# Kernel tuning notes

Hardware: AMD Instinct MI355X
Metric: run time of the kernel (lower is better)

## Reference

```python
import jax, jax.numpy as jnp
import numpy as np

B, N, D = 2, 2048, 1024
H, DH = 16, 64
THETA = 10000.0


def setup_inputs() -> dict:
    key = jax.random.key(0)
    k1, k2, k3, k4 = jax.random.split(key, 4)
    hidden_states = jax.random.normal(k1, (B, N, D), dtype=jnp.float32)
    # to_qkv: Linear(D, 3*H*DH, bias=False); stored as [in, out]
    w_qkv = jax.random.normal(k2, (D, 3 * H * DH), dtype=jnp.float32) * (1.0 / np.sqrt(D))
    # to_out: Linear(H*DH, D) with bias (torch default)
    w_out = jax.random.normal(k3, (H * DH, D), dtype=jnp.float32) * (1.0 / np.sqrt(H * DH))
    b_out = jax.random.normal(k4, (D,), dtype=jnp.float32) * 0.01
    return {"hidden_states": hidden_states, "w_qkv": w_qkv, "w_out": w_out, "b_out": b_out}


def _rope_cos_sin(n, dh, dtype):
    # lucidrains RotaryEmbedding: interleaved pairs, theta=10000
    inv_freq = 1.0 / (THETA ** (jnp.arange(0, dh, 2, dtype=jnp.float32) / dh))  # [dh/2]
    t = jnp.arange(n, dtype=jnp.float32)
    freqs = t[:, None] * inv_freq[None, :]                 # [n, dh/2]
    freqs = jnp.repeat(freqs, 2, axis=-1)                  # [n, dh] interleaved
    return jnp.cos(freqs).astype(dtype), jnp.sin(freqs).astype(dtype)


def _rotate_half(x):
    # interleaved: (..., d) -> pairs (x1, x2) -> (-x2, x1)
    x = x.reshape(*x.shape[:-1], -1, 2)
    x1, x2 = x[..., 0], x[..., 1]
    return jnp.stack([-x2, x1], axis=-1).reshape(*x.shape[:-2], -1)


def reference(hidden_states, w_qkv, w_out, b_out):
    b, n, d = hidden_states.shape
    qkv = hidden_states @ w_qkv                            # [b, n, 3*H*DH]
    q, k, v = jnp.split(qkv, 3, axis=-1)
    # b n (h d) -> b h n d
    to_heads = lambda t: t.reshape(b, n, H, DH).transpose(0, 2, 1, 3)
    q, k, v = to_heads(q), to_heads(k), to_heads(v)
    cos, sin = _rope_cos_sin(n, DH, q.dtype)               # [n, DH]
    q = q * cos + _rotate_half(q) * sin
    k = k * cos + _rotate_half(k) * sin
    scale = 1.0 / np.sqrt(DH)
    scores = jnp.einsum('bhqd,bhkd->bhqk', q, k) * scale   # [b, h, n, n]
    attn = jax.nn.softmax(scores, axis=-1)
    out = jnp.einsum('bhqk,bhkd->bhqd', attn, v)           # [b, h, n, DH]
    out = out.transpose(0, 2, 1, 3).reshape(b, n, H * DH)  # b h n d -> b n (h d)
    return out @ w_out + b_out
```

## Files before the change

### kernel.cpp

```cpp
#include <hip/hip_runtime.h>
#include <hip/hip_bf16.h>

typedef __bf16 bf16;
typedef unsigned int u32;
typedef __attribute__((ext_vector_type(4))) float f32x4;
typedef __attribute__((ext_vector_type(16))) float f32x16;
typedef __attribute__((ext_vector_type(8))) bf16 bf16x8;
typedef __attribute__((ext_vector_type(4))) bf16 bf16x4;
typedef __attribute__((ext_vector_type(2))) bf16 bf16x2;
typedef __attribute__((ext_vector_type(4))) u32 u32x4;
typedef __attribute__((ext_vector_type(2))) u32 u32x2;

#define GPTR(p) ((const __attribute__((address_space(1))) u32*)(p))
#define SPTR(p) ((__attribute__((address_space(3))) u32*)(p))

#if __has_builtin(__builtin_amdgcn_permlane32_swap)
#define HAVE_PLSWAP 1
#else
#define HAVE_PLSWAP 0
#endif
#if __has_builtin(__builtin_amdgcn_fdot2_f32_bf16)
#define HAVE_DOT2 1
#else
#define HAVE_DOT2 0
#endif

constexpr int BATCH = 2, SEQ = 2048, DMODEL = 1024, NH = 16, HD = 64, QKV3 = 3072;
constexpr int MTOK = BATCH * SEQ;

constexpr size_t OXB = 0;
constexpr size_t OWQ = OXB + (size_t)MTOK * DMODEL * 2;
constexpr size_t OWO = OWQ + (size_t)QKV3 * DMODEL * 2;
constexpr size_t OCS = OWO + (size_t)DMODEL * DMODEL * 2;
constexpr size_t OCQ = OCS + (size_t)SEQ * 32 * 8;
constexpr size_t OQR = OCQ + (size_t)MTOK * QKV3 * 2;
constexpr size_t OKR = OQR + (size_t)BATCH * NH * SEQ * HD * 2;
constexpr size_t OVT = OKR + (size_t)BATCH * NH * SEQ * HD * 2;
constexpr size_t OAO = OXB;

static __device__ __forceinline__ bf16 tobf(float x) { return (bf16)x; }
static __device__ __forceinline__ float tof(bf16 x) { return (float)x; }

static __device__ __forceinline__ f32x4 mfma16(bf16x8 a, bf16x8 b, f32x4 c) {
  return __builtin_amdgcn_mfma_f32_16x16x32_bf16(a, b, c, 0, 0, 0);
}
static __device__ __forceinline__ f32x16 mfma32(bf16x8 a, bf16x8 b, f32x16 c) {
  return __builtin_amdgcn_mfma_f32_32x32x16_bf16(a, b, c, 0, 0, 0);
}

__global__ void k_prep(const float* __restrict__ hs, const float* __restrict__ wqkv,
                       const float* __restrict__ wout, float* __restrict__ cs,
                       bf16* __restrict__ Xb, bf16* __restrict__ Wqkt,
                       bf16* __restrict__ Woutt) {
  __shared__ float tile[32][33];
  int blk = blockIdx.x, tid = threadIdx.x;
  if (blk < 256) {
    int idx = blk * 256 + tid;
    int n = idx >> 5, i = idx & 31;
    float freq = powf(10000.0f, -(float)(2 * i) / 64.0f);
    float ang = (float)n * freq;
    float s, c;
    sincosf(ang, &s, &c);
    cs[idx * 2] = c;
    cs[idx * 2 + 1] = s;
  } else if (blk < 256 + 4096) {
    int i = (blk - 256) * 256 + tid;
    float4 v = ((const float4*)hs)[i];
    bf16x4 o = {tobf(v.x), tobf(v.y), tobf(v.z), tobf(v.w)};
    ((bf16x4*)Xb)[i] = o;
  } else {
    const float* in;
    bf16* out;
    int R, C, n0, k0;
    if (blk < 256 + 4096 + 3072) {
      int t = blk - 4352;
      in = wqkv; out = Wqkt; R = DMODEL; C = QKV3;
      n0 = (t % 96) * 32; k0 = (t / 96) * 32;
    } else {
      int t = blk - 7424;
      in = wout; out = Woutt; R = DMODEL; C = DMODEL;
      n0 = (t & 31) * 32; k0 = (t >> 5) * 32;
    }
    int tx = tid & 31, ty = tid >> 5;
#pragma unroll
    for (int r = ty; r < 32; r += 8) tile[r][tx] = in[(size_t)(k0 + r) * C + n0 + tx];
    __syncthreads();
#pragma unroll
    for (int r = ty; r < 32; r += 8) out[(size_t)(n0 + r) * R + k0 + tx] = tobf(tile[tx][r]);
  }
}


__global__ __launch_bounds__(256) void k_gemm2(const bf16* __restrict__ A, const bf16* __restrict__ Bt,
                                               float* __restrict__ C, const float* __restrict__ bias,
                                               int M, int Nn, int K) {
  __shared__ __attribute__((aligned(16))) char smem[49152];
  const int nTn = Nn >> 7;
  int nwg = gridDim.x;
  int bid = blockIdx.x;
  int wgs = (bid & 7) * (nwg >> 3) + (bid >> 3);
  const int m0 = (wgs / nTn) << 7;
  const int n0 = (wgs % nTn) << 7;
  const int tid = threadIdx.x;
  const int lane = tid & 63, w = tid >> 6;
  const int wr = w >> 1, wc = w & 1;
  const int l15 = lane & 15, lhi = lane >> 4;
  f32x4 acc[4][4] = {};

  const int flat0 = w * 1024 + lane * 16;
  const int flat1 = flat0 + 4096;
  const int row0 = flat0 >> 6, ke0 = (flat0 & 63) >> 1;
  const int row1 = flat1 >> 6, ke1 = (flat1 & 63) >> 1;

#define GSTAGE(bb_, k0_)                                                                       \
  do {                                                                                         \
    __builtin_amdgcn_global_load_lds(GPTR(A + (size_t)(m0 + row0) * K + (k0_) + ke0),          \
                                     SPTR(smem + (bb_)*16384 + flat0), 16, 0, 0);              \
    __builtin_amdgcn_global_load_lds(GPTR(A + (size_t)(m0 + row1) * K + (k0_) + ke1),          \
                                     SPTR(smem + (bb_)*16384 + flat1), 16, 0, 0);              \
    __builtin_amdgcn_global_load_lds(GPTR(Bt + (size_t)(n0 + row0) * K + (k0_) + ke0),         \
                                     SPTR(smem + (bb_)*16384 + 8192 + flat0), 16, 0, 0);       \
    __builtin_amdgcn_global_load_lds(GPTR(Bt + (size_t)(n0 + row1) * K + (k0_) + ke1),         \
                                     SPTR(smem + (bb_)*16384 + 8192 + flat1), 16, 0, 0);       \
  } while (0)

  GSTAGE(0, 0);
  GSTAGE(1, 32);
  const int nIt = K >> 5;
  int bi = 0, b2 = 2;
  for (int it = 0; it < nIt; ++it) {
    if (it < nIt - 1) {
      asm volatile("s_waitcnt vmcnt(4)" ::: "memory");
    } else {
      asm volatile("s_waitcnt vmcnt(0)" ::: "memory");
    }
    __builtin_amdgcn_s_barrier();
    if (it + 2 < nIt) GSTAGE(b2, (it + 2) << 5);
    const bf16* As = (const bf16*)(smem + bi * 16384);
    const bf16* Bs = (const bf16*)(smem + bi * 16384 + 8192);
    bf16x8 af[4], bfv[4];
#pragma unroll
    for (int i = 0; i < 4; ++i) {
      af[i] = *(const bf16x8*)(As + (wr * 64 + i * 16 + l15) * 32 + lhi * 8);
      bfv[i] = *(const bf16x8*)(Bs + (wc * 64 + i * 16 + l15) * 32 + lhi * 8);
    }
    __builtin_amdgcn_s_setprio(1);
#pragma unroll
    for (int i = 0; i < 4; ++i)
#pragma unroll
      for (int j = 0; j < 4; ++j) acc[i][j] = mfma16(af[i], bfv[j], acc[i][j]);
    __builtin_amdgcn_s_setprio(0);
    bi = (bi == 2) ? 0 : bi + 1;
    b2 = (b2 == 2) ? 0 : b2 + 1;
  }
#undef GSTAGE

  float bj[4];
#pragma unroll
  for (int j = 0; j < 4; ++j) bj[j] = bias[n0 + wc * 64 + j * 16 + l15];
#pragma unroll
  for (int i = 0; i < 4; ++i)
#pragma unroll
    for (int j = 0; j < 4; ++j) {
      int row = m0 + wr * 64 + i * 16 + lhi * 4;
      int col = n0 + wc * 64 + j * 16 + l15;
#pragma unroll
      for (int r = 0; r < 4; ++r) C[(size_t)(row + r) * Nn + col] = acc[i][j][r] + bj[j];
    }
}


__global__ __launch_bounds__(256) void k_gemm1f(const bf16* __restrict__ A, const bf16* __restrict__ Bt,
                                                const float* __restrict__ cs,
                                                bf16* __restrict__ Qr, bf16* __restrict__ Kr,
                                                bf16* __restrict__ Vt) {
  constexpr int K = DMODEL, Nn = QKV3;
  __shared__ __attribute__((aligned(16))) char smem[49152];
  const int nTn = Nn >> 7;
  int nwg = gridDim.x;
  int bid = blockIdx.x;
  int wgs = (bid & 7) * (nwg >> 3) + (bid >> 3);
  const int m0 = (wgs / nTn) << 7;
  const int n0 = (wgs % nTn) << 7;
  const int tid = threadIdx.x;
  const int lane = tid & 63, w = tid >> 6;
  const int wr = w >> 1, wc = w & 1;
  const int l15 = lane & 15, lhi = lane >> 4;
  f32x4 acc[4][4] = {};

  const int flat0 = w * 1024 + lane * 16;
  const int flat1 = flat0 + 4096;
  const int row0 = flat0 >> 6, ke0 = (flat0 & 63) >> 1;
  const int row1 = flat1 >> 6, ke1 = (flat1 & 63) >> 1;

#define GSTAGE(bb_, k0_)                                                                       \
  do {                                                                                         \
    __builtin_amdgcn_global_load_lds(GPTR(A + (size_t)(m0 + row0) * K + (k0_) + ke0),          \
                                     SPTR(smem + (bb_)*16384 + flat0), 16, 0, 0);              \
    __builtin_amdgcn_global_load_lds(GPTR(A + (size_t)(m0 + row1) * K + (k0_) + ke1),          \
                                     SPTR(smem + (bb_)*16384 + flat1), 16, 0, 0);              \
    __builtin_amdgcn_global_load_lds(GPTR(Bt + (size_t)(n0 + row0) * K + (k0_) + ke0),         \
                                     SPTR(smem + (bb_)*16384 + 8192 + flat0), 16, 0, 0);       \
    __builtin_amdgcn_global_load_lds(GPTR(Bt + (size_t)(n0 + row1) * K + (k0_) + ke1),         \
                                     SPTR(smem + (bb_)*16384 + 8192 + flat1), 16, 0, 0);       \
  } while (0)

  GSTAGE(0, 0);
  GSTAGE(1, 32);
  const int nIt = K >> 5;
  int bi = 0, b2 = 2;
  for (int it = 0; it < nIt; ++it) {
    if (it < nIt - 1) {
      asm volatile("s_waitcnt vmcnt(4)" ::: "memory");
    } else {
      asm volatile("s_waitcnt vmcnt(0)" ::: "memory");
    }
    __builtin_amdgcn_s_barrier();
    if (it + 2 < nIt) GSTAGE(b2, (it + 2) << 5);
    const bf16* As = (const bf16*)(smem + bi * 16384);
    const bf16* Bs = (const bf16*)(smem + bi * 16384 + 8192);
    bf16x8 af[4], bfv[4];
#pragma unroll
    for (int i = 0; i < 4; ++i) {
      af[i] = *(const bf16x8*)(As + (wr * 64 + i * 16 + l15) * 32 + lhi * 8);
      bfv[i] = *(const bf16x8*)(Bs + (wc * 64 + i * 16 + l15) * 32 + lhi * 8);
    }
    __builtin_amdgcn_s_setprio(1);
#pragma unroll
    for (int i = 0; i < 4; ++i)
#pragma unroll
      for (int j = 0; j < 4; ++j) acc[i][j] = mfma16(af[i], bfv[j], acc[i][j]);
    __builtin_amdgcn_s_setprio(0);
    bi = (bi == 2) ? 0 : bi + 1;
    b2 = (b2 == 2) ? 0 : b2 + 1;
  }
#undef GSTAGE

  __syncthreads();
  const int part = n0 >> 10;
  const int b = m0 >> 11;

  if (part < 2) {
    bf16* Cs = (bf16*)smem;
#pragma unroll
    for (int i = 0; i < 4; ++i)
#pragma unroll
      for (int j = 0; j < 4; ++j) {
        int row = wr * 64 + i * 16 + lhi * 4;
        int col = wc * 64 + j * 16 + l15;
#pragma unroll
        for (int r = 0; r < 4; ++r) Cs[(row + r) * 128 + col] = tobf(acc[i][j][r]);
      }
    __syncthreads();
    bf16* dst = part == 0 ? Qr : Kr;
#pragma unroll
    for (int inst = 0; inst < 8; ++inst) {
      int flat = inst * 4096 + tid * 16;
      int row = flat >> 8, c0 = (flat & 255) >> 1;
      int n = (m0 + row) & 2047;
      int gc = (n0 & 1023) + c0;
      int h = gc >> 6, d0 = gc & 63;
      u32x4 v = *(const u32x4*)(smem + flat);
      const float* cp = cs + (((n << 5) + (d0 >> 1)) << 1);
      f32x4 csA = *(const f32x4*)cp;
      f32x4 csB = *(const f32x4*)(cp + 4);
      u32x4 ow;
#pragma unroll
      for (int j = 0; j < 4; ++j) {
        float cc = (j == 0) ? csA[0] : (j == 1) ? csA[2] : (j == 2) ? csB[0] : csB[2];
        float sn = (j == 0) ? csA[1] : (j == 1) ? csA[3] : (j == 2) ? csB[1] : csB[3];
        u32 pw = v[j];
        u32 tl = pw << 16, th = pw & 0xffff0000u;
        float a0, a1;
        __builtin_memcpy(&a0, &tl, 4);
        __builtin_memcpy(&a1, &th, 4);
        bf16 o0 = tobf(a0 * cc - a1 * sn);
        bf16 o1 = tobf(a1 * cc + a0 * sn);
        unsigned short u0, u1;
        __builtin_memcpy(&u0, &o0, 2);
        __builtin_memcpy(&u1, &o1, 2);
        ow[j] = (u32)u0 | ((u32)u1 << 16);
      }
      *(u32x4*)(dst + (((size_t)(b * 16 + h) * 2048 + n) << 6) + d0) = ow;
    }
  } else {
#pragma unroll
    for (int i = 0; i < 4; ++i)
#pragma unroll
      for (int j = 0; j < 4; ++j) {
        int col = wc * 64 + j * 16 + l15;
#pragma unroll
        for (int r = 0; r < 4; ++r) {
          int row = wr * 64 + i * 16 + lhi * 4 + r;
          int byte = (col << 8) + ((((row >> 3) ^ (col & 7)) << 4) | ((row & 7) << 1));
          *(bf16*)(smem + byte) = tobf(acc[i][j][r]);
        }
      }
    __syncthreads();
#pragma unroll
    for (int inst = 0; inst < 8; ++inst) {
      int flat = inst * 4096 + tid * 16;
      int c = flat >> 8;
      int rr0 = (flat & 255) >> 1;
      u32x4 vv = *(const u32x4*)(smem + (c << 8) + ((((rr0 >> 3) ^ (c & 7)) << 4)));
      int gc = (n0 & 1023) + c;
      int h = gc >> 6, dd = gc & 63;
      *(u32x4*)(Vt + (((size_t)(b * 16 + h) * 64 + dd) << 11) + (m0 & 2047) + rr0) = vv;
    }
  }
}

__global__ __launch_bounds__(512, 4) void k_attn(const bf16* __restrict__ Qr,
                                                 const bf16* __restrict__ Kr,
                                                 const bf16* __restrict__ Vt,
                                                 bf16* __restrict__ AO) {
  __shared__ __attribute__((aligned(16))) char lds[2][40960];
  int wg = blockIdx.x;
  int work = (wg & 7) * 64 + (wg >> 3);
  int qc = work & 15, h = (work >> 4) & 15, b = work >> 8;
  int tid = threadIdx.x;
  int wv = tid >> 6, lane = tid & 63;
  int pipe = wv >> 2, wsub = wv & 3;
  int l31 = lane & 31, h5 = lane >> 5;
  int q0 = qc * 128 + wsub * 32;
  int kbase = pipe << 10;
  const bf16* Qb = Qr + ((size_t)(b * NH + h)) * SEQ * 64;
  const bf16* Kb = Kr + ((size_t)(b * NH + h)) * SEQ * 64;
  const bf16* Vb = Vt + ((size_t)(b * NH + h)) * 64 * SEQ;
  char* pb = lds[pipe];

  int ptid = tid & 255;
  int sf0 = ptid * 16, sf1 = 4096 + ptid * 16;
  int sr0 = sf0 >> 7, sr1 = sf1 >> 7;
  int sc0 = (sf0 & 127) ^ ((sr0 & 7) << 4);
  int sc1 = (sf1 & 127) ^ ((sr1 & 7) << 4);
  size_t kgb0 = (size_t)sr0 * 64 + (sc0 >> 1), kgb1 = (size_t)sr1 * 64 + (sc1 >> 1);
  size_t vgb0 = (size_t)sr0 * SEQ + (sc0 >> 1), vgb1 = (size_t)sr1 * SEQ + (sc1 >> 1);

#define STAGE_K(bi_, kb_)                                                                     \
  do {                                                                                        \
    size_t ko_ = (size_t)(kbase + (kb_));                                                     \
    char* bb_ = pb + (bi_)*8192;                                                              \
    __builtin_amdgcn_global_load_lds(GPTR(Kb + ko_ * 64 + kgb0), SPTR(bb_ + sf0), 16, 0, 0);  \
    __builtin_amdgcn_global_load_lds(GPTR(Kb + ko_ * 64 + kgb1), SPTR(bb_ + sf1), 16, 0, 0);  \
  } while (0)
#define STAGE_V(bi_, kb_)                                                                     \
  do {                                                                                        \
    size_t ko_ = (size_t)(kbase + (kb_));                                                     \
    char* bb_ = pb + 24576 + (bi_)*8192;                                                      \
    __builtin_amdgcn_global_load_lds(GPTR(Vb + ko_ + vgb0), SPTR(bb_ + sf0), 16, 0, 0);       \
    __builtin_amdgcn_global_load_lds(GPTR(Vb + ko_ + vgb1), SPTR(bb_ + sf1), 16, 0, 0);       \
  } while (0)

  bf16x8 qf[4];
#pragma unroll
  for (int s = 0; s < 4; ++s) qf[s] = *(const bf16x8*)(Qb + (q0 + l31) * 64 + s * 16 + h5 * 8);

  f32x16 acc0 = {}, acc1 = {};
#if HAVE_DOT2
  float sacc0 = 0.f, sacc1 = 0.f, sacc2 = 0.f, sacc3 = 0.f;
  const bf16x2 ones2 = {(bf16)1.0f, (bf16)1.0f};
#else
  float ssum_run = 0.f;
#endif
  const float sc = 0.125f * 1.44269504f;
  const float FOFF = 8.0f;
  const int sw = (l31 & 7) << 4;
  const int cbase = h5 * 16;

  STAGE_K(0, 0);
  STAGE_V(0, 0);
  STAGE_K(1, 64);

  constexpr int NT = (SEQ / 2) / 64;
  int kc = 0, kc2 = 2;
  for (int t = 0; t < NT; ++t) {
    if (t < NT - 1) {
      asm volatile("s_waitcnt vmcnt(2)" ::: "memory");
    } else {
      asm volatile("s_waitcnt vmcnt(0)" ::: "memory");
    }
    __builtin_amdgcn_s_barrier();
    if (t + 1 < NT) STAGE_V((t + 1) & 1, (t + 1) * 64);
    if (t + 2 < NT) STAGE_K(kc2, (t + 2) * 64);
    char* cbK = pb + kc * 8192;
    char* cbV = pb + 24576 + (t & 1) * 8192;
    kc = (kc == 2) ? 0 : kc + 1;
    kc2 = (kc2 == 2) ? 0 : kc2 + 1;

    f32x16 st0 = {}, st1 = {};
    __builtin_amdgcn_s_setprio(1);
#pragma unroll
    for (int s = 0; s < 4; ++s) {
      bf16x8 kf0 = *(const bf16x8*)(cbK + l31 * 128 + ((s * 32 + cbase) ^ sw));
      bf16x8 kf1 = *(const bf16x8*)(cbK + 4096 + l31 * 128 + ((s * 32 + cbase) ^ sw));
      st0 = mfma32(kf0, qf[s], st0);
      st1 = mfma32(kf1, qf[s], st1);
    }
    __builtin_amdgcn_s_setprio(0);

    float p[32];
#pragma unroll
    for (int r = 0; r < 16; ++r) p[r] = __builtin_amdgcn_exp2f(fmaf(st0[r], sc, -FOFF));
#pragma unroll
    for (int r = 0; r < 16; ++r) p[16 + r] = __builtin_amdgcn_exp2f(fmaf(st1[r], sc, -FOFF));

    u32 P32[16];
#pragma unroll
    for (int i = 0; i < 16; ++i) {
      bf16 lo = tobf(p[2 * i]), hi = tobf(p[2 * i + 1]);
      unsigned short ul, uh;
      __builtin_memcpy(&ul, &lo, 2);
      __builtin_memcpy(&uh, &hi, 2);
      P32[i] = (u32)ul | ((u32)uh << 16);
    }

#if HAVE_DOT2
#pragma unroll
    for (int i = 0; i < 16; i += 4) {
      sacc0 = __builtin_amdgcn_fdot2_f32_bf16(__builtin_bit_cast(bf16x2, P32[i]), ones2, sacc0, false);
      sacc1 = __builtin_amdgcn_fdot2_f32_bf16(__builtin_bit_cast(bf16x2, P32[i + 1]), ones2, sacc1, false);
      sacc2 = __builtin_amdgcn_fdot2_f32_bf16(__builtin_bit_cast(bf16x2, P32[i + 2]), ones2, sacc2, false);
      sacc3 = __builtin_amdgcn_fdot2_f32_bf16(__builtin_bit_cast(bf16x2, P32[i + 3]), ones2, sacc3, false);
    }
#else
    {
      float sm[16];
#pragma unroll
      for (int i = 0; i < 16; ++i) {
        u32 ulo = P32[i] << 16, uhi = P32[i] & 0xffff0000u;
        float flo, fhi;
        __builtin_memcpy(&flo, &ulo, 4);
        __builtin_memcpy(&fhi, &uhi, 4);
        sm[i] = flo + fhi;
      }
#pragma unroll
      for (int off = 8; off > 0; off >>= 1)
#pragma unroll
        for (int r = 0; r < off; ++r) sm[r] += sm[r + off];
      ssum_run += sm[0];
    }
#endif

#if !HAVE_PLSWAP
    const int evens[8] = {0, 1, 4, 5, 8, 9, 12, 13};
    const int odds[8] = {2, 3, 6, 7, 10, 11, 14, 15};
    u32 recv[8];
#pragma unroll
    for (int j = 0; j < 8; ++j) {
      u32 sv = h5 ? P32[evens[j]] : P32[odds[j]];
      recv[j] = (u32)__shfl_xor((int)sv, 32, 64);
    }
#endif

    __builtin_amdgcn_s_setprio(1);
#pragma unroll
    for (int s2 = 0; s2 < 4; ++s2) {
      int x0 = ((s2 >> 1) << 3) + ((s2 & 1) << 2);
#if HAVE_PLSWAP
      u32x2 r02 = __builtin_amdgcn_permlane32_swap(P32[x0], P32[x0 + 2], false, false);
      u32x2 r13 = __builtin_amdgcn_permlane32_swap(P32[x0 + 1], P32[x0 + 3], false, false);
      u32x4 wv4 = {r02.x, r13.x, r02.y, r13.y};
#else
      u32 w0 = h5 ? recv[2 * s2] : P32[x0];
      u32 w1 = h5 ? recv[2 * s2 + 1] : P32[x0 + 1];
      u32 w2 = h5 ? P32[x0 + 2] : recv[2 * s2];
      u32 w3 = h5 ? P32[x0 + 3] : recv[2 * s2 + 1];
      u32x4 wv4 = {w0, w1, w2, w3};
#endif
      bf16x8 pfr = __builtin_bit_cast(bf16x8, wv4);
      bf16x8 vf0 = *(const bf16x8*)(cbV + l31 * 128 + ((s2 * 32 + cbase) ^ sw));
      bf16x8 vf1 = *(const bf16x8*)(cbV + 4096 + l31 * 128 + ((s2 * 32 + cbase) ^ sw));
      acc0 = mfma32(vf0, pfr, acc0);
      acc1 = mfma32(vf1, pfr, acc1);
    }
    __builtin_amdgcn_s_setprio(0);
  }

#if HAVE_DOT2
  float ssum = (sacc0 + sacc1) + (sacc2 + sacc3);
#else
  float ssum = ssum_run;
#endif

  __syncthreads();
  float* cacc = (float*)&lds[0][0];
  float* csum = (float*)(&lds[0][0] + 36864);
  int slot = (wsub * 64 + lane) * 36;
  if (pipe == 1) {
#pragma unroll
    for (int r = 0; r < 16; r += 4) {
      *(f32x4*)(cacc + slot + r) = f32x4{acc0[r], acc0[r + 1], acc0[r + 2], acc0[r + 3]};
      *(f32x4*)(cacc + slot + 16 + r) = f32x4{acc1[r], acc1[r + 1], acc1[r + 2], acc1[r + 3]};
    }
    csum[wsub * 64 + lane] = ssum;
  }
  __syncthreads();
  if (pipe == 0) {
#pragma unroll
    for (int r = 0; r < 16; r += 4) {
      f32x4 v0 = *(const f32x4*)(cacc + slot + r);
      f32x4 v1 = *(const f32x4*)(cacc + slot + 16 + r);
#pragma unroll
      for (int j = 0; j < 4; ++j) { acc0[r + j] += v0[j]; acc1[r + j] += v1[j]; }
    }
    ssum += csum[wsub * 64 + lane];
    ssum += __shfl_xor(ssum, 32, 64);
    float inv = 1.0f / ssum;
    size_t tok = (size_t)(b * SEQ + q0 + l31);
#pragma unroll
    for (int a = 0; a < 4; ++a) {
      bf16x4 ov0, ov1;
#pragma unroll
      for (int j = 0; j < 4; ++j) {
        ov0[j] = tobf(acc0[4 * a + j] * inv);
        ov1[j] = tobf(acc1[4 * a + j] * inv);
      }
      *(bf16x4*)(AO + tok * (NH * HD) + h * 64 + 8 * a + 4 * h5) = ov0;
      *(bf16x4*)(AO + tok * (NH * HD) + h * 64 + 32 + 8 * a + 4 * h5) = ov1;
    }
  }
#undef STAGE_K
#undef STAGE_V
}


extern "C" void kernel_launch(void* const* d_in, const int* in_sizes, int n_in,
                              void* d_out, int out_size, void* d_ws, size_t ws_size,
                              hipStream_t stream) {
  const float* hs = (const float*)d_in[0];
  const float* wqkv = (const float*)d_in[1];
  const float* wout = (const float*)d_in[2];
  const float* bout = (const float*)d_in[3];
  char* ws = (char*)d_ws;
  bf16* Xb = (bf16*)(ws + OXB);
  bf16* Wqkt = (bf16*)(ws + OWQ);
  bf16* Woutt = (bf16*)(ws + OWO);
  float* cs = (float*)(ws + OCS);
  bf16* Qr = (bf16*)(ws + OQR);
  bf16* Kr = (bf16*)(ws + OKR);
  bf16* Vt = (bf16*)(ws + OVT);
  bf16* AO = (bf16*)(ws + OAO);

  k_prep<<<8448, 256, 0, stream>>>(hs, wqkv, wout, cs, Xb, Wqkt, Woutt);
  k_gemm1f<<<(MTOK / 128) * (QKV3 / 128), 256, 0, stream>>>(Xb, Wqkt, cs, Qr, Kr, Vt);
  k_attn<<<BATCH * NH * (SEQ / 128), 512, 0, stream>>>(Qr, Kr, Vt, AO);
  k_gemm2<<<(MTOK / 128) * (DMODEL / 128), 256, 0, stream>>>(AO, Woutt, (float*)d_out, bout, MTOK, DMODEL, DMODEL);
}
```

Measured before the change: 117.6 us.

## Swizzle GEMM LDS layout and move w_out transpose into QKV GEMM launch

Applies an XOR swizzle to the 16-byte chunks of each LDS row in both GEMM kernels, at the global-to-LDS write and at the fragment read, to reduce LDS bank conflicts. Moves the w_out fp32->bf16 transpose out of the prep kernel into extra trailing blocks of the QKV GEMM launch. This shortens the prep kernel's critical path and lets the transpose overlap the GEMM tail. It adds index arithmetic, and the extra blocks enlarge the GEMM grid.

Result: no change. 116.2 us (-1.2%).

```diff
diff --git a/kernel.cpp b/kernel.cpp
--- a/kernel.cpp
+++ b/kernel.cpp
@@ -49,9 +49,8 @@
 }
 
 __global__ void k_prep(const float* __restrict__ hs, const float* __restrict__ wqkv,
-                       const float* __restrict__ wout, float* __restrict__ cs,
-                       bf16* __restrict__ Xb, bf16* __restrict__ Wqkt,
-                       bf16* __restrict__ Woutt) {
+                       float* __restrict__ cs, bf16* __restrict__ Xb,
+                       bf16* __restrict__ Wqkt) {
   __shared__ float tile[32][33];
   int blk = blockIdx.x, tid = threadIdx.x;
   if (blk < 256) {
@@ -69,26 +68,17 @@
     bf16x4 o = {tobf(v.x), tobf(v.y), tobf(v.z), tobf(v.w)};
     ((bf16x4*)Xb)[i] = o;
   } else {
-    const float* in;
-    bf16* out;
-    int R, C, n0, k0;
-    if (blk < 256 + 4096 + 3072) {
-      int t = blk - 4352;
-      in = wqkv; out = Wqkt; R = DMODEL; C = QKV3;
-      n0 = (t % 96) * 32; k0 = (t / 96) * 32;
-    } else {
-      int t = blk - 7424;
-      in = wout; out = Woutt; R = DMODEL; C = DMODEL;
-      n0 = (t & 31) * 32; k0 = (t >> 5) * 32;
-    }
+    int t = blk - 4352;
+    int n0 = (t % 96) * 32, k0 = (t / 96) * 32;
     int tx = tid & 31, ty = tid >> 5;
 #pragma unroll
-    for (int r = ty; r < 32; r += 8) tile[r][tx] = in[(size_t)(k0 + r) * C + n0 + tx];
+    for (int r = ty; r < 32; r += 8) tile[r][tx] = wqkv[(size_t)(k0 + r) * QKV3 + n0 + tx];
     __syncthreads();
 #pragma unroll
-    for (int r = ty; r < 32; r += 8) out[(size_t)(n0 + r) * R + k0 + tx] = tobf(tile[tx][r]);
-  }
-}
+    for (int r = ty; r < 32; r += 8) Wqkt[(size_t)(n0 + r) * DMODEL + k0 + tx] = tobf(tile[tx][r]);
+  }
+}
+
 
 
 __global__ __launch_bounds__(256) void k_gemm2(const bf16* __restrict__ A, const bf16* __restrict__ Bt,
@@ -109,8 +99,10 @@
 
   const int flat0 = w * 1024 + lane * 16;
   const int flat1 = flat0 + 4096;
-  const int row0 = flat0 >> 6, ke0 = (flat0 & 63) >> 1;
-  const int row1 = flat1 >> 6, ke1 = (flat1 & 63) >> 1;
+  const int row0 = flat0 >> 6, row1 = flat1 >> 6;
+  const int ke0 = (((flat0 & 63) >> 4) ^ ((row0 >> 1) & 3)) << 3;
+  const int ke1 = (((flat1 & 63) >> 4) ^ ((row1 >> 1) & 3)) << 3;
+  const int rsw = ((l15 >> 1) & 3) << 3;
 
 #define GSTAGE(bb_, k0_)                                                                       \
   do {                                                                                         \
@@ -141,8 +133,8 @@
     bf16x8 af[4], bfv[4];
 #pragma unroll
     for (int i = 0; i < 4; ++i) {
-      af[i] = *(const bf16x8*)(As + (wr * 64 + i * 16 + l15) * 32 + lhi * 8);
-      bfv[i] = *(const bf16x8*)(Bs + (wc * 64 + i * 16 + l15) * 32 + lhi * 8);
+      af[i] = *(const bf16x8*)(As + (wr * 64 + i * 16 + l15) * 32 + ((lhi << 3) ^ rsw));
+      bfv[i] = *(const bf16x8*)(Bs + (wc * 64 + i * 16 + l15) * 32 + ((lhi << 3) ^ rsw));
     }
     __builtin_amdgcn_s_setprio(1);
 #pragma unroll
@@ -172,17 +164,32 @@
 
 __global__ __launch_bounds__(256) void k_gemm1f(const bf16* __restrict__ A, const bf16* __restrict__ Bt,
                                                 const float* __restrict__ cs,
+                                                const float* __restrict__ wout, bf16* __restrict__ Woutt,
                                                 bf16* __restrict__ Qr, bf16* __restrict__ Kr,
                                                 bf16* __restrict__ Vt) {
   constexpr int K = DMODEL, Nn = QKV3;
+  constexpr int NG = (MTOK / 128) * (QKV3 / 128);
   __shared__ __attribute__((aligned(16))) char smem[49152];
+  int bid = blockIdx.x;
+  const int tid = threadIdx.x;
+
+  if (bid >= NG) {
+    float* tile = (float*)smem;
+    int t = bid - NG;
+    int n0 = (t & 31) * 32, k0 = (t >> 5) * 32;
+    int tx = tid & 31, ty = tid >> 5;
+#pragma unroll
+    for (int r = ty; r < 32; r += 8) tile[r * 33 + tx] = wout[(size_t)(k0 + r) * DMODEL + n0 + tx];
+    __syncthreads();
+#pragma unroll
+    for (int r = ty; r < 32; r += 8) Woutt[(size_t)(n0 + r) * DMODEL + k0 + tx] = tobf(tile[tx * 33 + r]);
+    return;
+  }
+
   const int nTn = Nn >> 7;
-  int nwg = gridDim.x;
-  int bid = blockIdx.x;
-  int wgs = (bid & 7) * (nwg >> 3) + (bid >> 3);
+  int wgs = (bid & 7) * (NG >> 3) + (bid >> 3);
   const int m0 = (wgs / nTn) << 7;
   const int n0 = (wgs % nTn) << 7;
-  const int tid = threadIdx.x;
   const int lane = tid & 63, w = tid >> 6;
   const int wr = w >> 1, wc = w & 1;
   const int l15 = lane & 15, lhi = lane >> 4;
@@ -190,8 +197,10 @@
 
   const int flat0 = w * 1024 + lane * 16;
   const int flat1 = flat0 + 4096;
-  const int row0 = flat0 >> 6, ke0 = (flat0 & 63) >> 1;
-  const int row1 = flat1 >> 6, ke1 = (flat1 & 63) >> 1;
+  const int row0 = flat0 >> 6, row1 = flat1 >> 6;
+  const int ke0 = (((flat0 & 63) >> 4) ^ ((row0 >> 1) & 3)) << 3;
+  const int ke1 = (((flat1 & 63) >> 4) ^ ((row1 >> 1) & 3)) << 3;
+  const int rsw = ((l15 >> 1) & 3) << 3;
 
 #define GSTAGE(bb_, k0_)                                                                       \
   do {                                                                                         \
@@ -222,8 +231,8 @@
     bf16x8 af[4], bfv[4];
 #pragma unroll
     for (int i = 0; i < 4; ++i) {
-      af[i] = *(const bf16x8*)(As + (wr * 64 + i * 16 + l15) * 32 + lhi * 8);
-      bfv[i] = *(const bf16x8*)(Bs + (wc * 64 + i * 16 + l15) * 32 + lhi * 8);
+      af[i] = *(const bf16x8*)(As + (wr * 64 + i * 16 + l15) * 32 + ((lhi << 3) ^ rsw));
+      bfv[i] = *(const bf16x8*)(Bs + (wc * 64 + i * 16 + l15) * 32 + ((lhi << 3) ^ rsw));
     }
     __builtin_amdgcn_s_setprio(1);
 #pragma unroll
@@ -542,8 +551,8 @@
   bf16* Vt = (bf16*)(ws + OVT);
   bf16* AO = (bf16*)(ws + OAO);
 
-  k_prep<<<8448, 256, 0, stream>>>(hs, wqkv, wout, cs, Xb, Wqkt, Woutt);
-  k_gemm1f<<<(MTOK / 128) * (QKV3 / 128), 256, 0, stream>>>(Xb, Wqkt, cs, Qr, Kr, Vt);
+  k_prep<<<7424, 256, 0, stream>>>(hs, wqkv, cs, Xb, Wqkt);
+  k_gemm1f<<<(MTOK / 128) * (QKV3 / 128) + 1024, 256, 0, stream>>>(Xb, Wqkt, cs, wout, Woutt, Qr, Kr, Vt);
   k_attn<<<BATCH * NH * (SEQ / 128), 512, 0, stream>>>(Qr, Kr, Vt, AO);
   k_gemm2<<<(MTOK / 128) * (DMODEL / 128), 256, 0, stream>>>(AO, Woutt, (float*)d_out, bout, MTOK, DMODEL, DMODEL);
 }
```
